# Kernel optimization log

Hardware: AMD Instinct MI355X
Metric: run time of the kernel (lower is better)

The kernel has to match this reference:

```python
import jax, jax.numpy as jnp
import numpy as np

C, T, H, W, K = 12, 10, 4, 7, 3  # hardcoded in the original forward
PAD = 1
EPS = 1e-5


def setup_inputs() -> dict:
    key = jax.random.key(0)
    ks = jax.random.split(key, 14)
    nt = 32768
    x = jax.random.normal(ks[0], (nt, C, T, H * W), jnp.float32)
    # G: Linear(T -> 2T) -> BN1d(2T) -> ReLU -> Linear(2T -> K) -> Softmax
    w_g1 = jax.random.normal(ks[1], (2 * T, T), jnp.float32) * 0.3
    g1_gamma = 1.0 + 0.1 * jax.random.normal(ks[2], (2 * T,), jnp.float32)
    g1_beta = 0.1 * jax.random.normal(ks[3], (2 * T,), jnp.float32)
    g1_mean = 0.1 * jax.random.normal(ks[4], (2 * T,), jnp.float32)
    g1_var = jax.random.uniform(ks[5], (2 * T,), jnp.float32, 0.5, 1.5)
    w_g2 = jax.random.normal(ks[6], (K, 2 * T), jnp.float32) * 0.3
    # L: Conv1d(C -> C//4, K) -> BN1d(C//4) -> ReLU -> Conv1d(C//4 -> C, 1) -> Sigmoid
    w_l1 = jax.random.normal(ks[7], (C // 4, C, K), jnp.float32) * 0.3
    l1_gamma = 1.0 + 0.1 * jax.random.normal(ks[8], (C // 4,), jnp.float32)
    l1_beta = 0.1 * jax.random.normal(ks[9], (C // 4,), jnp.float32)
    l1_mean = 0.1 * jax.random.normal(ks[10], (C // 4,), jnp.float32)
    l1_var = jax.random.uniform(ks[11], (C // 4,), jnp.float32, 0.5, 1.5)
    w_l2 = jax.random.normal(ks[12], (C, C // 4, 1), jnp.float32) * 0.3
    return dict(x=x, w_g1=w_g1, g1_gamma=g1_gamma, g1_beta=g1_beta,
                g1_mean=g1_mean, g1_var=g1_var, w_g2=w_g2, w_l1=w_l1,
                l1_gamma=l1_gamma, l1_beta=l1_beta, l1_mean=l1_mean,
                l1_var=l1_var, w_l2=w_l2)


def reference(x, w_g1, g1_gamma, g1_beta, g1_mean, g1_var, w_g2,
              w_l1, l1_gamma, l1_beta, l1_mean, l1_var, w_l2):
    n = x.shape[0]
    new_x = x.reshape(n, C, T, H, W)
    # adaptive_avg_pool2d((1,1)) == mean over spatial dims -> [n, C, T]
    pooled = new_x.mean(axis=(3, 4))
    # --- G branch: per-(sample,channel) temporal kernel, [n, C, K] ---
    rows = pooled.reshape(n * C, T)
    z = rows @ w_g1.T
    z = (z - g1_mean) * jax.lax.rsqrt(g1_var + EPS) * g1_gamma + g1_beta
    z = jax.nn.relu(z)
    kern = jax.nn.softmax(z @ w_g2.T, axis=-1).reshape(n, C, K)
    # --- L branch: local channel-temporal gating, [n, C, T] ---
    a = jax.lax.conv_general_dilated(pooled, w_l1, (1,), [(K // 2, K // 2)],
                                     dimension_numbers=('NCH', 'OIH', 'NCH'))
    a = (a - l1_mean[None, :, None]) * jax.lax.rsqrt(l1_var + EPS)[None, :, None] \
        * l1_gamma[None, :, None] + l1_beta[None, :, None]
    a = jax.nn.relu(a)
    a = jax.lax.conv_general_dilated(a, w_l2, (1,), [(0, 0)],
                                     dimension_numbers=('NCH', 'OIH', 'NCH'))
    act = jax.nn.sigmoid(a)  # [n, C, T]
    # --- modulate and apply per-(sample,channel) depthwise temporal conv ---
    xm = new_x * act[:, :, :, None, None]  # [n, C, T, H, W]
    xp = jnp.pad(xm, ((0, 0), (0, 0), (PAD, PAD), (0, 0), (0, 0)))
    out = kern[:, :, 0, None, None, None] * xp[:, :, 0:T]
    for j in range(1, K):  # K=3, tiny structural loop
        out = out + kern[:, :, j, None, None, None] * xp[:, :, j:j + T]
    # permute [n,c,t,h,w] -> [n,t,c,h,w] and flatten time into batch
    out = jnp.transpose(out, (0, 2, 1, 3, 4)).reshape(n * T, C, H, W)
    return out
```

## Files before the change

kernel.cpp:

```cpp
#include <hip/hip_runtime.h>


#define CC 12
#define TT 10
#define SAMPLE 3360
#define SAMPLE4 840
#define EPSF 1e-5f

typedef float f4 __attribute__((ext_vector_type(4)));

__global__ __launch_bounds__(256) void tam_kernel(
    const float* __restrict__ x,
    const float* __restrict__ w_g1,
    const float* __restrict__ g1_gamma, const float* __restrict__ g1_beta,
    const float* __restrict__ g1_mean,  const float* __restrict__ g1_var,
    const float* __restrict__ w_g2,
    const float* __restrict__ w_l1,
    const float* __restrict__ l1_gamma, const float* __restrict__ l1_beta,
    const float* __restrict__ l1_mean,  const float* __restrict__ l1_var,
    const float* __restrict__ w_l2,
    float* __restrict__ out)
{
    __shared__ f4    sx4[SAMPLE4];
    __shared__ float spool[120];
    __shared__ float sz[240];
    __shared__ float sa1[30];
    __shared__ float skern[36];
    __shared__ float sact[120];
    __shared__ float wg1s[200], wg2s[60], wl1s[108], wl2s[36];
    __shared__ float gs[20], gb[20], lsc[3], lbi[3];

    const int n    = blockIdx.x;
    const int tid  = threadIdx.x;
    const int wid  = tid >> 6;
    const int lane = tid & 63;

    const f4* xg = reinterpret_cast<const f4*>(x + (size_t)n * SAMPLE);
    for (int i = wid; i < 13; i += 4) {
        __builtin_amdgcn_global_load_lds(
            (const __attribute__((address_space(1))) void*)(xg + i * 64 + lane),
            (__attribute__((address_space(3))) void*)(&sx4[i * 64]),
            16, 0, 0);
    }
    if (tid < 8) sx4[832 + tid] = xg[832 + tid];

    for (int i = tid; i < 200; i += 256) wg1s[i] = w_g1[i];
    if (tid < 60)  wg2s[tid] = w_g2[tid];
    if (tid < 108) wl1s[tid] = w_l1[tid];
    if (tid < 36)  wl2s[tid] = w_l2[tid];
    if (tid < 20) {
        const float s = rsqrtf(g1_var[tid] + EPSF) * g1_gamma[tid];
        gs[tid] = s; gb[tid] = g1_beta[tid] - g1_mean[tid] * s;
    } else if (tid < 23) {
        const int m = tid - 20;
        const float s = rsqrtf(l1_var[m] + EPSF) * l1_gamma[m];
        lsc[m] = s; lbi[m] = l1_beta[m] - l1_mean[m] * s;
    }
    __syncthreads();

    if (tid < 120) {
        const f4* rp = sx4 + tid * 7;
        f4 a = rp[0];
        #pragma unroll
        for (int i = 1; i < 7; ++i) a += rp[i];
        spool[tid] = (a.x + a.y + a.z + a.w) * (1.0f / 28.0f);
    }
    __syncthreads();

    for (int task = tid; task < 270; task += 256) {
        if (task < 240) {
            const int c = task / 20, j = task % 20;
            float s = 0.f;
            #pragma unroll
            for (int t = 0; t < TT; ++t)
                s += spool[c * TT + t] * wg1s[j * TT + t];
            sz[task] = fmaxf(gs[j] * s + gb[j], 0.f);
        } else {
            const int e = task - 240;
            const int m = e / TT, t = e % TT;
            float s = 0.f;
            #pragma unroll
            for (int c = 0; c < CC; ++c) {
                #pragma unroll
                for (int k = 0; k < 3; ++k) {
                    const int t2 = t + k - 1;
                    if (t2 >= 0 && t2 < TT)
                        s += spool[c * TT + t2] * wl1s[(m * CC + c) * 3 + k];
                }
            }
            sa1[e] = fmaxf(lsc[m] * s + lbi[m], 0.f);
        }
    }
    __syncthreads();

    if (tid < CC) {
        const int c = tid;
        float sc0 = 0.f, sc1 = 0.f, sc2 = 0.f;
        #pragma unroll
        for (int j = 0; j < 20; ++j) {
            const float zj = sz[c * 20 + j];
            sc0 += zj * wg2s[j];
            sc1 += zj * wg2s[20 + j];
            sc2 += zj * wg2s[40 + j];
        }
        const float mx = fmaxf(sc0, fmaxf(sc1, sc2));
        const float e0 = __expf(sc0 - mx), e1 = __expf(sc1 - mx), e2 = __expf(sc2 - mx);
        const float ri = 1.0f / (e0 + e1 + e2);
        skern[c]      = e0 * ri;
        skern[12 + c] = e1 * ri;
        skern[24 + c] = e2 * ri;
    }
    if (tid >= 64 && tid < 64 + 120) {
        const int idx = tid - 64;
        const int c = idx / TT, t = idx % TT;
        float s = 0.f;
        #pragma unroll
        for (int m = 0; m < 3; ++m) s += sa1[m * TT + t] * wl2s[c * 3 + m];
        sact[idx] = 1.0f / (1.0f + __expf(-s));
    }
    __syncthreads();

    f4* og = reinterpret_cast<f4*>(out + (size_t)n * SAMPLE);
    for (int v = tid; v < SAMPLE4; v += 256) {
        const int t   = v / 84;
        const int rem = v % 84;
        const int c   = rem / 7;
        const int s4  = rem % 7;
        const int base = c * 70 + s4;
        const float k0 = skern[c];
        const float k1 = skern[12 + c];
        const float k2 = skern[24 + c];
        f4 acc = (k1 * sact[c * TT + t]) * sx4[base + t * 7];
        if (t > 0)
            acc += (k0 * sact[c * TT + t - 1]) * sx4[base + (t - 1) * 7];
        if (t < TT - 1)
            acc += (k2 * sact[c * TT + t + 1]) * sx4[base + (t + 1) * 7];
        __builtin_nontemporal_store(acc, og + v);
    }
}

extern "C" void kernel_launch(void* const* d_in, const int* in_sizes, int n_in,
                              void* d_out, int out_size, void* d_ws, size_t ws_size,
                              hipStream_t stream) {
    (void)n_in; (void)out_size; (void)d_ws; (void)ws_size;
    const float* x        = (const float*)d_in[0];
    const float* w_g1     = (const float*)d_in[1];
    const float* g1_gamma = (const float*)d_in[2];
    const float* g1_beta  = (const float*)d_in[3];
    const float* g1_mean  = (const float*)d_in[4];
    const float* g1_var   = (const float*)d_in[5];
    const float* w_g2     = (const float*)d_in[6];
    const float* w_l1     = (const float*)d_in[7];
    const float* l1_gamma = (const float*)d_in[8];
    const float* l1_beta  = (const float*)d_in[9];
    const float* l1_mean  = (const float*)d_in[10];
    const float* l1_var   = (const float*)d_in[11];
    const float* w_l2     = (const float*)d_in[12];
    float* out = (float*)d_out;

    const int n_total = in_sizes[0] / SAMPLE;
    tam_kernel<<<n_total, 256, 0, stream>>>(
        x, w_g1, g1_gamma, g1_beta, g1_mean, g1_var, w_g2,
        w_l1, l1_gamma, l1_beta, l1_mean, l1_var, w_l2, out);
}
```

Baseline: 191.4 us.

## Shrink blocks to 128 threads and read small weights directly from global

Halves the block size to 128 threads and reassigns the load, pooling, MLP and output loops to fit the smaller block. The shared-memory copies of the tiny weight and BN parameters are removed, and those values are read straight from global (cached) memory, with BN folding recomputed inline. sact now reuses the spool buffer, and the output loop is fully unrolled. The aim is less LDS and less per-block setup so more blocks fit per CU, at the cost of repeated scalar global loads and redundant rsqrt work.

Measured after the change: 193.6 us. Within noise of the previous version (+1.1%).

```diff
diff --git a/kernel.cpp b/kernel.cpp
--- a/kernel.cpp
+++ b/kernel.cpp
@@ -9,7 +9,7 @@
 
 typedef float f4 __attribute__((ext_vector_type(4)));
 
-__global__ __launch_bounds__(256) void tam_kernel(
+__global__ __launch_bounds__(128) void tam_kernel(
     const float* __restrict__ x,
     const float* __restrict__ w_g1,
     const float* __restrict__ g1_gamma, const float* __restrict__ g1_beta,
@@ -26,9 +26,6 @@
     __shared__ float sz[240];
     __shared__ float sa1[30];
     __shared__ float skern[36];
-    __shared__ float sact[120];
-    __shared__ float wg1s[200], wg2s[60], wl1s[108], wl2s[36];
-    __shared__ float gs[20], gb[20], lsc[3], lbi[3];
 
     const int n    = blockIdx.x;
     const int tid  = threadIdx.x;
@@ -36,26 +33,13 @@
     const int lane = tid & 63;
 
     const f4* xg = reinterpret_cast<const f4*>(x + (size_t)n * SAMPLE);
-    for (int i = wid; i < 13; i += 4) {
+    for (int i = wid; i < 13; i += 2) {
         __builtin_amdgcn_global_load_lds(
             (const __attribute__((address_space(1))) void*)(xg + i * 64 + lane),
             (__attribute__((address_space(3))) void*)(&sx4[i * 64]),
             16, 0, 0);
     }
     if (tid < 8) sx4[832 + tid] = xg[832 + tid];
-
-    for (int i = tid; i < 200; i += 256) wg1s[i] = w_g1[i];
-    if (tid < 60)  wg2s[tid] = w_g2[tid];
-    if (tid < 108) wl1s[tid] = w_l1[tid];
-    if (tid < 36)  wl2s[tid] = w_l2[tid];
-    if (tid < 20) {
-        const float s = rsqrtf(g1_var[tid] + EPSF) * g1_gamma[tid];
-        gs[tid] = s; gb[tid] = g1_beta[tid] - g1_mean[tid] * s;
-    } else if (tid < 23) {
-        const int m = tid - 20;
-        const float s = rsqrtf(l1_var[m] + EPSF) * l1_gamma[m];
-        lsc[m] = s; lbi[m] = l1_beta[m] - l1_mean[m] * s;
-    }
     __syncthreads();
 
     if (tid < 120) {
@@ -67,14 +51,15 @@
     }
     __syncthreads();
 
-    for (int task = tid; task < 270; task += 256) {
+    for (int task = tid; task < 270; task += 128) {
         if (task < 240) {
             const int c = task / 20, j = task % 20;
             float s = 0.f;
             #pragma unroll
             for (int t = 0; t < TT; ++t)
-                s += spool[c * TT + t] * wg1s[j * TT + t];
-            sz[task] = fmaxf(gs[j] * s + gb[j], 0.f);
+                s += spool[c * TT + t] * w_g1[j * TT + t];
+            const float rs = rsqrtf(g1_var[j] + EPSF);
+            sz[task] = fmaxf((s - g1_mean[j]) * rs * g1_gamma[j] + g1_beta[j], 0.f);
         } else {
             const int e = task - 240;
             const int m = e / TT, t = e % TT;
@@ -85,23 +70,25 @@
                 for (int k = 0; k < 3; ++k) {
                     const int t2 = t + k - 1;
                     if (t2 >= 0 && t2 < TT)
-                        s += spool[c * TT + t2] * wl1s[(m * CC + c) * 3 + k];
+                        s += spool[c * TT + t2] * w_l1[(m * CC + c) * 3 + k];
                 }
             }
-            sa1[e] = fmaxf(lsc[m] * s + lbi[m], 0.f);
+            const float rs = rsqrtf(l1_var[m] + EPSF);
+            sa1[e] = fmaxf((s - l1_mean[m]) * rs * l1_gamma[m] + l1_beta[m], 0.f);
         }
     }
     __syncthreads();
 
-    if (tid < CC) {
-        const int c = tid;
+    float* sact = spool;
+    if (tid >= 116) {
+        const int c = tid - 116;
         float sc0 = 0.f, sc1 = 0.f, sc2 = 0.f;
         #pragma unroll
         for (int j = 0; j < 20; ++j) {
             const float zj = sz[c * 20 + j];
-            sc0 += zj * wg2s[j];
-            sc1 += zj * wg2s[20 + j];
-            sc2 += zj * wg2s[40 + j];
+            sc0 += zj * w_g2[j];
+            sc1 += zj * w_g2[20 + j];
+            sc2 += zj * w_g2[40 + j];
         }
         const float mx = fmaxf(sc0, fmaxf(sc1, sc2));
         const float e0 = __expf(sc0 - mx), e1 = __expf(sc1 - mx), e2 = __expf(sc2 - mx);
@@ -110,32 +97,35 @@
         skern[12 + c] = e1 * ri;
         skern[24 + c] = e2 * ri;
     }
-    if (tid >= 64 && tid < 64 + 120) {
-        const int idx = tid - 64;
-        const int c = idx / TT, t = idx % TT;
+    if (tid < 120) {
+        const int c = tid / TT, t = tid % TT;
         float s = 0.f;
         #pragma unroll
-        for (int m = 0; m < 3; ++m) s += sa1[m * TT + t] * wl2s[c * 3 + m];
-        sact[idx] = 1.0f / (1.0f + __expf(-s));
+        for (int m = 0; m < 3; ++m) s += sa1[m * TT + t] * w_l2[c * 3 + m];
+        sact[tid] = 1.0f / (1.0f + __expf(-s));
     }
     __syncthreads();
 
     f4* og = reinterpret_cast<f4*>(out + (size_t)n * SAMPLE);
-    for (int v = tid; v < SAMPLE4; v += 256) {
-        const int t   = v / 84;
-        const int rem = v % 84;
-        const int c   = rem / 7;
-        const int s4  = rem % 7;
-        const int base = c * 70 + s4;
-        const float k0 = skern[c];
-        const float k1 = skern[12 + c];
-        const float k2 = skern[24 + c];
-        f4 acc = (k1 * sact[c * TT + t]) * sx4[base + t * 7];
-        if (t > 0)
-            acc += (k0 * sact[c * TT + t - 1]) * sx4[base + (t - 1) * 7];
-        if (t < TT - 1)
-            acc += (k2 * sact[c * TT + t + 1]) * sx4[base + (t + 1) * 7];
-        __builtin_nontemporal_store(acc, og + v);
+    #pragma unroll
+    for (int k = 0; k < 7; ++k) {
+        const int v = tid + k * 128;
+        if (k < 6 || tid < 72) {
+            const int t   = v / 84;
+            const int rem = v % 84;
+            const int c   = rem / 7;
+            const int s4  = rem % 7;
+            const int base = c * 70 + s4;
+            const float k0 = skern[c];
+            const float k1 = skern[12 + c];
+            const float k2 = skern[24 + c];
+            f4 acc = (k1 * sact[c * TT + t]) * sx4[base + t * 7];
+            if (t > 0)
+                acc += (k0 * sact[c * TT + t - 1]) * sx4[base + (t - 1) * 7];
+            if (t < TT - 1)
+                acc += (k2 * sact[c * TT + t + 1]) * sx4[base + (t + 1) * 7];
+            __builtin_nontemporal_store(acc, og + v);
+        }
     }
 }
 
@@ -159,7 +149,7 @@
     float* out = (float*)d_out;
 
     const int n_total = in_sizes[0] / SAMPLE;
-    tam_kernel<<<n_total, 256, 0, stream>>>(
+    tam_kernel<<<n_total, 128, 0, stream>>>(
         x, w_g1, g1_gamma, g1_beta, g1_mean, g1_var, w_g2,
         w_l1, l1_gamma, l1_beta, l1_mean, l1_var, w_l2, out);
 }
```
